# Kernel optimization log

Measured on AMD Instinct MI355X. Metric: run time of the kernel, lower is better.

Reference implementation:

```python
import jax, jax.numpy as jnp
import numpy as np

NUM_NODES = 2048
NUM_FEATURES = 512
NUM_CLASSES = 128
INF = 1e9  # finite stand-in for float('inf'): identical shortest-path results on
           # connected positive-weight graphs, but keeps gradients NaN-free


def bellman_ford(adj_matrix, source_node):
    """Min-plus Bellman-Ford relaxation.

    Returns:
      distances:    (N, N) where distances[v, i] = shortest dist source->v using <= i edges
      predecessors: (N,)   argmin predecessor on the final relaxation
      has_negative_cycle: () bool, True if an N-th relaxation still improves
    """
    n = adj_matrix.shape[0]
    init = jnp.full((n,), INF, dtype=adj_matrix.dtype).at[source_node].set(0.0)

    def step(dist, _):
        # new[v] = min(dist[v], min_u dist[u] + w(u, v))  -- one relaxation sweep
        new = jnp.minimum(dist, jnp.min(dist[:, None] + adj_matrix, axis=0))
        return new, new

    step = jax.checkpoint(step)  # O(N) saved state per step instead of O(N^2)
    final, hist = jax.lax.scan(step, init, None, length=n - 1)

    distances = jnp.concatenate([init[:, None], hist.T], axis=1)  # (N, N)

    relax = jnp.min(final[:, None] + adj_matrix, axis=0)
    predecessors = jnp.where(relax <= final,
                             jnp.argmin(final[:, None] + adj_matrix, axis=0),
                             -1)
    has_negative_cycle = jnp.any(jnp.minimum(final, relax) < final)
    return distances, predecessors, has_negative_cycle


def setup_inputs() -> dict:
    key = jax.random.key(0)
    k1, k2, k3 = jax.random.split(key, 3)
    adj_matrix = jax.random.uniform(k1, (NUM_NODES, NUM_NODES), dtype=jnp.float32)
    node_embedding = jax.random.normal(k2, (NUM_NODES, NUM_FEATURES), dtype=jnp.float32)
    fc_weight = jax.random.normal(k3, (NUM_CLASSES, NUM_FEATURES + NUM_NODES), dtype=jnp.float32) * 0.02
    fc_bias = jnp.zeros((NUM_CLASSES,), dtype=jnp.float32)
    return {
        "adj_matrix": adj_matrix,
        "node_embedding": node_embedding,
        "fc_weight": fc_weight,
        "fc_bias": fc_bias,
        "source_node": 0,
    }


def reference(adj_matrix, node_embedding, fc_weight, fc_bias, source_node):
    distances, predecessors, has_negative_cycle = bellman_ford(adj_matrix, source_node)
    # node_embedding plays the role of Embedding(arange(N)) lookup = full table
    node_features = jnp.concatenate([node_embedding, distances], axis=1)  # (N, F+N)
    output = node_features @ fc_weight.T + fc_bias  # (N, C)
    return output, has_negative_cycle
```

## Files before the change

### kernel.cpp

```cpp
#include <hip/hip_runtime.h>

#define NN   2048
#define FF   512
#define CC   128
#define WROW 2560
#define INFV 1.0e9f
#define NB   128
#define NT   1024
#define BN   16
#define HCAP 96

#define AL64(p)   __hip_atomic_load((p),  __ATOMIC_RELAXED, __HIP_MEMORY_SCOPE_AGENT)
#define AS64(p,v) __hip_atomic_store((p), (v), __ATOMIC_RELAXED, __HIP_MEMORY_SCOPE_AGENT)

struct WS {
    unsigned long long D[2][NN];
    unsigned long long Suf[CC][8];
};

__device__ __forceinline__ unsigned long long pk(unsigned tag, float v) {
    return ((unsigned long long)tag << 32) | (unsigned long long)__float_as_uint(v);
}
__device__ __forceinline__ unsigned tg(unsigned long long e) { return (unsigned)(e >> 32); }
__device__ __forceinline__ float    vl(unsigned long long e) { return __uint_as_float((unsigned)e); }

__global__ __launch_bounds__(NT, 1)
void bf_lean(const float* __restrict__ adj,
             const float* __restrict__ emb,
             const float* __restrict__ W,
             const float* __restrict__ bias,
             const int*   __restrict__ srcp,
             float*       __restrict__ out,
             WS* ws, int out_size)
{
    __shared__ __align__(16) float adjT[BN * NN];
    __shared__ __align__(16) float dist[NN];
    __shared__ float hist[HCAP][BN];
    __shared__ float red16[BN];

    const int tid = threadIdx.x;
    const int b   = blockIdx.x;
    const int src = *srcp;
    const int q   = (b & 7) * 16 + (b >> 3);
    const int vb  = q * BN;

    if (tid < BN)
        AS64(&ws->D[0][vb + tid], pk(0u, ((vb + tid) == src) ? 0.0f : INFV));

    #pragma unroll
    for (int it = 0; it < 8; ++it) {
        int r = tid + NT * it;
        int u = r >> 2, qc = (r & 3) * 4;
        float4 a = *(const float4*)(adj + (size_t)u * NN + vb + qc);
        adjT[(qc + 0) * NN + u] = a.x;
        adjT[(qc + 1) * NN + u] = a.y;
        adjT[(qc + 2) * NN + u] = a.z;
        adjT[(qc + 3) * NN + u] = a.w;
    }
    __syncthreads();

    const int vown = tid >> 6;
    const int lane = tid & 63;
    const int c0 = 2 * lane, c1 = c0 + 1;
    float p0 = (tid == src) ? 0.0f : INFV;
    float p1 = ((tid + NT) == src) ? 0.0f : INFV;

    float acc0, acc1;
    { float d0 = ((vb + vown) == src) ? 0.0f : INFV;
      acc0 = d0 * W[(size_t)c0 * WROW + FF];
      acc1 = d0 * W[(size_t)c1 * WROW + FF]; }

    int kconv = -1, hneg = 0;

    for (int s = 1; s <= NN; ++s) {
        const int pp = (s - 1) & 1;
        const unsigned want = (unsigned)(s - 1);
        unsigned long long e0 = AL64(&ws->D[pp][tid]);
        while (tg(e0) != want) { __builtin_amdgcn_s_sleep(1); e0 = AL64(&ws->D[pp][tid]); }
        unsigned long long e1 = AL64(&ws->D[pp][tid + NT]);
        while (tg(e1) != want) { __builtin_amdgcn_s_sleep(1); e1 = AL64(&ws->D[pp][tid + NT]); }
        float n0 = vl(e0), n1 = vl(e1);
        int ch = (n0 != p0) | (n1 != p1);
        p0 = n0; p1 = n1;
        dist[tid] = n0; dist[tid + NT] = n1;
        int any = __syncthreads_or(ch);
        if (s >= 2 && !any) { kconv = s - 1; break; }

        float m = 4.0e9f;
        const float* ar = adjT + vown * NN;
        #pragma unroll
        for (int k = 0; k < 8; ++k) {
            int u = 4 * lane + 256 * k;
            float4 dd = *(const float4*)(dist + u);
            float4 aa = *(const float4*)(ar + u);
            m = fminf(m, fminf(fminf(dd.x + aa.x, dd.y + aa.y),
                               fminf(dd.z + aa.z, dd.w + aa.w)));
        }
        #pragma unroll
        for (int st = 1; st < 64; st <<= 1) m = fminf(m, __shfl_xor(m, st, 64));
        float nv = fminf(dist[vb + vown], m);

        if (lane == 0) {
            AS64(&ws->D[s & 1][vb + vown], pk((unsigned)s, nv));
            if (s <= HCAP) hist[s - 1][vown] = nv;
        }
        if (s > HCAP && s < NN) {
            acc0 = fmaf(nv, W[(size_t)c0 * WROW + FF + s], acc0);
            acc1 = fmaf(nv, W[(size_t)c1 * WROW + FF + s], acc1);
        }
        __syncthreads();
    }

    if (kconv < 0) {
        unsigned long long e0 = AL64(&ws->D[0][tid]);
        while (tg(e0) != (unsigned)NN) { __builtin_amdgcn_s_sleep(1); e0 = AL64(&ws->D[0][tid]); }
        unsigned long long e1 = AL64(&ws->D[0][tid + NT]);
        while (tg(e1) != (unsigned)NN) { __builtin_amdgcn_s_sleep(1); e1 = AL64(&ws->D[0][tid + NT]); }
        int ch = (vl(e0) != p0) | (vl(e1) != p1);
        hneg = __syncthreads_or(ch) ? 1 : 0;
    } else if (kconv >= 1 && kconv <= NN - 2) {
        float ssum = 0.0f;
        for (int i = kconv + 1 + tid; i <= NN - 1; i += NT)
            ssum += W[(size_t)b * WROW + FF + i];
        #pragma unroll
        for (int st = 1; st < 64; st <<= 1) ssum += __shfl_xor(ssum, st, 64);
        if (lane == 0) red16[vown] = ssum;
        __syncthreads();
        if (tid == 0) {
            float x = 0.0f;
            #pragma unroll
            for (int w = 0; w < BN; ++w) x += red16[w];
            AS64(&ws->Suf[b][0], pk(0x40000000u + (unsigned)kconv, x));
        }
        const unsigned wantS = 0x40000000u + (unsigned)kconv;
        unsigned long long s0 = AL64(&ws->Suf[c0][0]);
        while (tg(s0) != wantS) { __builtin_amdgcn_s_sleep(1); s0 = AL64(&ws->Suf[c0][0]); }
        unsigned long long s1 = AL64(&ws->Suf[c1][0]);
        while (tg(s1) != wantS) { __builtin_amdgcn_s_sleep(1); s1 = AL64(&ws->Suf[c1][0]); }
        float dv = dist[vb + vown];
        acc0 = fmaf(dv, vl(s0), acc0);
        acc1 = fmaf(dv, vl(s1), acc1);
    }

    {
        int fmax = (kconv < 0) ? (NN - 1) : kconv;
        if (fmax > HCAP) fmax = HCAP;
        for (int s2 = 1; s2 <= fmax; ++s2) {
            float dv = hist[s2 - 1][vown];
            acc0 = fmaf(dv, W[(size_t)c0 * WROW + FF + s2], acc0);
            acc1 = fmaf(dv, W[(size_t)c1 * WROW + FF + s2], acc1);
        }
    }

    const int vE = vb + (tid & 15);
    const int cE = (2 * (tid >> 4)) & 127;
    float ea0 = 0.0f, ea1 = 0.0f;
    for (int chk = 0; chk < 16; ++chk) {
        int i0 = 32 * chk;
        const float4* ep = (const float4*)(emb + (size_t)vE * FF + i0);
        const float4* wa = (const float4*)(W + (size_t)cE * WROW + i0);
        const float4* wb = (const float4*)(W + (size_t)(cE + 1) * WROW + i0);
        #pragma unroll
        for (int j = 0; j < 8; ++j) {
            float4 e = ep[j], x = wa[j], y = wb[j];
            ea0 += e.x*x.x + e.y*x.y + e.z*x.z + e.w*x.w;
            ea1 += e.x*y.x + e.y*y.y + e.z*y.z + e.w*y.w;
        }
    }

    __syncthreads();
    float* comb = adjT;
    comb[(tid & 15) * 129 + cE]     = ea0;
    comb[(tid & 15) * 129 + cE + 1] = ea1;
    __syncthreads();
    float o0 = acc0 + comb[vown * 129 + c0] + bias[c0];
    float o1 = acc1 + comb[vown * 129 + c1] + bias[c1];
    *(float2*)(out + (size_t)(vb + vown) * CC + c0) = make_float2(o0, o1);
    if (b == 0 && tid == 0 && out_size > NN * CC)
        out[NN * CC] = hneg ? 1.0f : 0.0f;
}

extern "C" void kernel_launch(void* const* d_in, const int* in_sizes, int n_in,
                              void* d_out, int out_size, void* d_ws, size_t ws_size,
                              hipStream_t stream) {
    const float* adj  = (const float*)d_in[0];
    const float* emb  = (const float*)d_in[1];
    const float* W    = (const float*)d_in[2];
    const float* bias = (const float*)d_in[3];
    const int*   srcp = (const int*)d_in[4];
    float* outp = (float*)d_out;
    WS* ws = (WS*)d_ws;
    int osz = out_size;

    bf_lean<<<dim3(NB), dim3(NT), 0, stream>>>(adj, emb, W, bias, srcp,
                                               outp, ws, osz);
}
```

Measured before the change: 151.2 us.

## Replicate distance broadcast buffer across 8 copies and carry change flags in tags

Each block now writes its new distances to eight replicated global buffers, and each block polls only the replica chosen by its index. This spreads polling traffic from 128 blocks over more cache lines. A per-entry change bit is packed into the tag, so convergence detection no longer keeps previous values in registers. Shared dist is double-buffered to remove the trailing __syncthreads per step, and each thread now reads two adjacent entries. The cost is eight times as many global stores per step, plus more tag bookkeeping.

```diff
diff --git a/kernel.cpp b/kernel.cpp
--- a/kernel.cpp
+++ b/kernel.cpp
@@ -8,33 +8,36 @@
 #define NB   128
 #define NT   1024
 #define BN   16
+#define NR   8
 #define HCAP 96
 
 #define AL64(p)   __hip_atomic_load((p),  __ATOMIC_RELAXED, __HIP_MEMORY_SCOPE_AGENT)
 #define AS64(p,v) __hip_atomic_store((p), (v), __ATOMIC_RELAXED, __HIP_MEMORY_SCOPE_AGENT)
 
 struct WS {
-    unsigned long long D[2][NN];
+    unsigned long long D[2][NR][NN];
     unsigned long long Suf[CC][8];
 };
 
 __device__ __forceinline__ unsigned long long pk(unsigned tag, float v) {
     return ((unsigned long long)tag << 32) | (unsigned long long)__float_as_uint(v);
 }
-__device__ __forceinline__ unsigned tg(unsigned long long e) { return (unsigned)(e >> 32); }
-__device__ __forceinline__ float    vl(unsigned long long e) { return __uint_as_float((unsigned)e); }
+__device__ __forceinline__ unsigned stag(unsigned long long e) {
+    return (unsigned)(e >> 32) & 0x3FFFFFFFu;
+}
+__device__ __forceinline__ float vl(unsigned long long e) { return __uint_as_float((unsigned)e); }
 
 __global__ __launch_bounds__(NT, 1)
-void bf_lean(const float* __restrict__ adj,
-             const float* __restrict__ emb,
-             const float* __restrict__ W,
-             const float* __restrict__ bias,
-             const int*   __restrict__ srcp,
-             float*       __restrict__ out,
-             WS* ws, int out_size)
+void bf_mcast(const float* __restrict__ adj,
+              const float* __restrict__ emb,
+              const float* __restrict__ W,
+              const float* __restrict__ bias,
+              const int*   __restrict__ srcp,
+              float*       __restrict__ out,
+              WS* ws, int out_size)
 {
     __shared__ __align__(16) float adjT[BN * NN];
-    __shared__ __align__(16) float dist[NN];
+    __shared__ __align__(16) float dist2[2][NN];
     __shared__ float hist[HCAP][BN];
     __shared__ float red16[BN];
 
@@ -43,9 +46,14 @@
     const int src = *srcp;
     const int q   = (b & 7) * 16 + (b >> 3);
     const int vb  = q * BN;
-
-    if (tid < BN)
-        AS64(&ws->D[0][vb + tid], pk(0u, ((vb + tid) == src) ? 0.0f : INFV));
+    const int rep = b & (NR - 1);
+
+    if (tid < BN) {
+        float iv = ((vb + tid) == src) ? 0.0f : INFV;
+        unsigned long long w = pk(0u | (1u << 30), iv);
+        #pragma unroll
+        for (int r = 0; r < NR; ++r) AS64(&ws->D[0][r][vb + tid], w);
+    }
 
     #pragma unroll
     for (int it = 0; it < 8; ++it) {
@@ -62,9 +70,6 @@
     const int vown = tid >> 6;
     const int lane = tid & 63;
     const int c0 = 2 * lane, c1 = c0 + 1;
-    float p0 = (tid == src) ? 0.0f : INFV;
-    float p1 = ((tid + NT) == src) ? 0.0f : INFV;
-
     float acc0, acc1;
     { float d0 = ((vb + vown) == src) ? 0.0f : INFV;
       acc0 = d0 * W[(size_t)c0 * WROW + FF];
@@ -73,50 +78,56 @@
     int kconv = -1, hneg = 0;
 
     for (int s = 1; s <= NN; ++s) {
-        const int pp = (s - 1) & 1;
+        const int p = (s - 1) & 1;
         const unsigned want = (unsigned)(s - 1);
-        unsigned long long e0 = AL64(&ws->D[pp][tid]);
-        while (tg(e0) != want) { __builtin_amdgcn_s_sleep(1); e0 = AL64(&ws->D[pp][tid]); }
-        unsigned long long e1 = AL64(&ws->D[pp][tid + NT]);
-        while (tg(e1) != want) { __builtin_amdgcn_s_sleep(1); e1 = AL64(&ws->D[pp][tid + NT]); }
-        float n0 = vl(e0), n1 = vl(e1);
-        int ch = (n0 != p0) | (n1 != p1);
-        p0 = n0; p1 = n1;
-        dist[tid] = n0; dist[tid + NT] = n1;
+        unsigned long long* Dq = &ws->D[p][rep][0];
+        unsigned long long e0 = AL64(&Dq[2 * tid]);
+        unsigned long long e1 = AL64(&Dq[2 * tid + 1]);
+        while (stag(e0) != want) { __builtin_amdgcn_s_sleep(2); e0 = AL64(&Dq[2 * tid]); }
+        while (stag(e1) != want) { __builtin_amdgcn_s_sleep(2); e1 = AL64(&Dq[2 * tid + 1]); }
+        int ch = (int)(((e0 | e1) >> 62) & 1ull);
+        dist2[p][2 * tid]     = vl(e0);
+        dist2[p][2 * tid + 1] = vl(e1);
         int any = __syncthreads_or(ch);
         if (s >= 2 && !any) { kconv = s - 1; break; }
 
         float m = 4.0e9f;
         const float* ar = adjT + vown * NN;
+        const float* dd0 = &dist2[p][0];
         #pragma unroll
         for (int k = 0; k < 8; ++k) {
             int u = 4 * lane + 256 * k;
-            float4 dd = *(const float4*)(dist + u);
+            float4 dd = *(const float4*)(dd0 + u);
             float4 aa = *(const float4*)(ar + u);
             m = fminf(m, fminf(fminf(dd.x + aa.x, dd.y + aa.y),
                                fminf(dd.z + aa.z, dd.w + aa.w)));
         }
         #pragma unroll
         for (int st = 1; st < 64; st <<= 1) m = fminf(m, __shfl_xor(m, st, 64));
-        float nv = fminf(dist[vb + vown], m);
+        float own = dist2[p][vb + vown];
+        float nv = fminf(own, m);
 
         if (lane == 0) {
-            AS64(&ws->D[s & 1][vb + vown], pk((unsigned)s, nv));
+            unsigned ch_own = (nv != own) ? 1u : 0u;
+            unsigned long long w = pk((unsigned)s | (ch_own << 30), nv);
+            unsigned long long* Dn = &ws->D[s & 1][0][0];
+            #pragma unroll
+            for (int r = 0; r < NR; ++r) AS64(&Dn[r * NN + vb + vown], w);
             if (s <= HCAP) hist[s - 1][vown] = nv;
         }
         if (s > HCAP && s < NN) {
             acc0 = fmaf(nv, W[(size_t)c0 * WROW + FF + s], acc0);
             acc1 = fmaf(nv, W[(size_t)c1 * WROW + FF + s], acc1);
         }
-        __syncthreads();
     }
 
     if (kconv < 0) {
-        unsigned long long e0 = AL64(&ws->D[0][tid]);
-        while (tg(e0) != (unsigned)NN) { __builtin_amdgcn_s_sleep(1); e0 = AL64(&ws->D[0][tid]); }
-        unsigned long long e1 = AL64(&ws->D[0][tid + NT]);
-        while (tg(e1) != (unsigned)NN) { __builtin_amdgcn_s_sleep(1); e1 = AL64(&ws->D[0][tid + NT]); }
-        int ch = (vl(e0) != p0) | (vl(e1) != p1);
+        unsigned long long* Dq = &ws->D[0][rep][0];
+        unsigned long long e0 = AL64(&Dq[2 * tid]);
+        unsigned long long e1 = AL64(&Dq[2 * tid + 1]);
+        while (stag(e0) != (unsigned)NN) { __builtin_amdgcn_s_sleep(2); e0 = AL64(&Dq[2 * tid]); }
+        while (stag(e1) != (unsigned)NN) { __builtin_amdgcn_s_sleep(2); e1 = AL64(&Dq[2 * tid + 1]); }
+        int ch = (int)(((e0 | e1) >> 62) & 1ull);
         hneg = __syncthreads_or(ch) ? 1 : 0;
     } else if (kconv >= 1 && kconv <= NN - 2) {
         float ssum = 0.0f;
@@ -130,18 +141,19 @@
             float x = 0.0f;
             #pragma unroll
             for (int w = 0; w < BN; ++w) x += red16[w];
-            AS64(&ws->Suf[b][0], pk(0x40000000u + (unsigned)kconv, x));
-        }
-        const unsigned wantS = 0x40000000u + (unsigned)kconv;
+            AS64(&ws->Suf[b][0], pk(0x3F000000u + (unsigned)kconv, x));
+        }
+        const unsigned wantS = 0x3F000000u + (unsigned)kconv;
         unsigned long long s0 = AL64(&ws->Suf[c0][0]);
-        while (tg(s0) != wantS) { __builtin_amdgcn_s_sleep(1); s0 = AL64(&ws->Suf[c0][0]); }
+        while (stag(s0) != wantS) { __builtin_amdgcn_s_sleep(2); s0 = AL64(&ws->Suf[c0][0]); }
         unsigned long long s1 = AL64(&ws->Suf[c1][0]);
-        while (tg(s1) != wantS) { __builtin_amdgcn_s_sleep(1); s1 = AL64(&ws->Suf[c1][0]); }
-        float dv = dist[vb + vown];
+        while (stag(s1) != wantS) { __builtin_amdgcn_s_sleep(2); s1 = AL64(&ws->Suf[c1][0]); }
+        float dv = dist2[kconv & 1][vb + vown];
         acc0 = fmaf(dv, vl(s0), acc0);
         acc1 = fmaf(dv, vl(s1), acc1);
     }
 
+    __syncthreads();
     {
         int fmax = (kconv < 0) ? (NN - 1) : kconv;
         if (fmax > HCAP) fmax = HCAP;
@@ -192,6 +204,6 @@
     WS* ws = (WS*)d_ws;
     int osz = out_size;
 
-    bf_lean<<<dim3(NB), dim3(NT), 0, stream>>>(adj, emb, W, bias, srcp,
-                                               outp, ws, osz);
-}
+    bf_mcast<<<dim3(NB), dim3(NT), 0, stream>>>(adj, emb, W, bias, srcp,
+                                                outp, ws, osz);
+}
```

New measurement: 195.7 us. 1.29x slower.
